# Performance work log

Measured on AMD Instinct MI355X. Metric: run time of the kernel, lower is better.

The kernel has to match this reference:

```python
import jax, jax.numpy as jnp
import numpy as np

B, S, H, DH = 2, 2048, 24, 32
E = H * DH  # 768


def setup_inputs() -> dict:
    key = jax.random.key(0)
    ks = jax.random.split(key, 7)
    embedding = jax.random.normal(ks[0], (B, S, E), dtype=jnp.float32)
    mask = jax.random.randint(ks[1], (B, S, S), 0, 2).astype(bool)
    # per-head QKV weights (applied as x @ W, equivalent param to torch Linear W.T)
    Wq = jax.random.normal(ks[2], (H, DH, DH), dtype=jnp.float32) * 0.05
    Wk = jax.random.normal(ks[3], (H, DH, DH), dtype=jnp.float32) * 0.05
    Wv = jax.random.normal(ks[4], (H, DH, DH), dtype=jnp.float32) * 0.05
    Wo = jax.random.normal(ks[5], (E, E), dtype=jnp.float32) * 0.02
    bo = jax.random.normal(ks[6], (E,), dtype=jnp.float32) * 0.02
    return {"embedding": embedding, "mask": mask, "Wq": Wq, "Wk": Wk,
            "Wv": Wv, "Wo": Wo, "bo": bo}


def reference(embedding, mask, Wq, Wk, Wv, Wo, bo):
    # split channels into heads: [B,S,H,DH]
    xh = embedding.reshape(B, S, H, DH)
    # per-head projections (batched over heads)
    Q = jnp.einsum('bshd,hde->bhse', xh, Wq)
    K = jnp.einsum('bshd,hde->bhse', xh, Wk)
    V = jnp.einsum('bshd,hde->bhse', xh, Wv)
    scale = 1.0 / jnp.sqrt(jnp.float32(DH))
    scores = jnp.einsum('bhqd,bhkd->bhqk', Q, K) * scale
    # faithful quirk: masked positions set to -1e-6 (not -inf)
    scores = jnp.where(mask[:, None, :, :], scores, jnp.float32(-1e-6))
    probs = jax.nn.softmax(scores, axis=-1)
    out = jnp.einsum('bhqk,bhkd->bqhd', probs, V)  # [B,S,H,DH]
    out = out.reshape(B, S, E)  # concat heads along feature dim
    return out @ Wo.T + bo
```

## Files before the change

kernel.cpp:

```cpp
#include <hip/hip_runtime.h>
#include <hip/hip_bf16.h>

#define B_  2
#define S_  2048
#define H_  24
#define DH_ 32
#define E_  768
#define SW_ (S_/32)

#define NB_QKV  ((S_/64)*(B_*H_))
#define NB_MASK ((B_*S_*S_)/256)
#define NB_WO   ((E_*E_)/1024)

typedef __attribute__((ext_vector_type(8))) short short8;
typedef __attribute__((ext_vector_type(4))) float f32x4;
typedef _Float16 half8  __attribute__((ext_vector_type(8)));
typedef _Float16 half2v __attribute__((ext_vector_type(2)));
typedef __fp16   fp16x2 __attribute__((ext_vector_type(2)));

static __device__ __forceinline__ half2v cvt2h(float a, float b) {
    fp16x2 t = __builtin_amdgcn_cvt_pkrtz(a, b);
    return __builtin_bit_cast(half2v, t);
}

static __device__ __forceinline__ short4 pack4(float a, float b, float c, float d) {
    union { __hip_bfloat162 h[2]; short4 s; } u;
    u.h[0] = __float22bfloat162_rn(make_float2(a, b));
    u.h[1] = __float22bfloat162_rn(make_float2(c, d));
    return u.s;
}
static __device__ __forceinline__ short8 pack8f(const float* a, const float* b) {
    union { __hip_bfloat162 h[4]; short8 s; } u;
    u.h[0] = __float22bfloat162_rn(make_float2(a[0], a[1]));
    u.h[1] = __float22bfloat162_rn(make_float2(a[2], a[3]));
    u.h[2] = __float22bfloat162_rn(make_float2(b[0], b[1]));
    u.h[3] = __float22bfloat162_rn(make_float2(b[2], b[3]));
    return u.s;
}
static __device__ __forceinline__ short8 pack8(float4 a, float4 b) {
    union { __hip_bfloat162 h[4]; short8 s; } u;
    u.h[0] = __float22bfloat162_rn(make_float2(a.x, a.y));
    u.h[1] = __float22bfloat162_rn(make_float2(a.z, a.w));
    u.h[2] = __float22bfloat162_rn(make_float2(b.x, b.y));
    u.h[3] = __float22bfloat162_rn(make_float2(b.z, b.w));
    return u.s;
}
static __device__ __forceinline__ short8 wfrag(const float* __restrict__ Wb,
                                               int quad, int eo) {
    float w[8];
#pragma unroll
    for (int j = 0; j < 8; ++j) w[j] = Wb[(quad * 8 + j) * 32 + eo];
    return pack8f(w, w + 4);
}

#define QSCALE  0.25503487f

static __device__ __forceinline__ float mexp2(float s, unsigned mw, int pos) {
    const int m = __builtin_amdgcn_sbfe((int)mw, pos, 1);
    const int xi = __builtin_bit_cast(int, s) & m;
    return __builtin_amdgcn_exp2f(__builtin_bit_cast(float, xi));
}

__global__ __launch_bounds__(256) void prep_qkv_kernel(
    const float* __restrict__ x, const int* __restrict__ mask,
    const float* __restrict__ Wo,
    const float* __restrict__ Wq, const float* __restrict__ Wk,
    const float* __restrict__ Wv,
    __hip_bfloat16* __restrict__ Qo,
    __hip_bfloat16* __restrict__ Ko,
    _Float16* __restrict__ Vto,
    unsigned int* __restrict__ mbits, _Float16* __restrict__ Wob)
{
    const int bx = blockIdx.x;
    if (bx < NB_QKV) {
        const int bh   = bx >> 5;
        const int b    = bh / H_;
        const int h    = bh - b * H_;
        const int wave = threadIdx.x >> 6;
        const int lane = threadIdx.x & 63;
        const int col  = lane & 15;
        const int quad = lane >> 4;
        const int sw   = (bx & 31) * 64 + wave * 16;
        const int s    = sw + col;

        const float* xp = x + ((size_t)b * S_ + s) * E_ + h * DH_ + quad * 8;
        const float4 xa = *reinterpret_cast<const float4*>(xp);
        const float4 xb = *reinterpret_cast<const float4*>(xp + 4);
        const short8 xf = pack8(xa, xb);

        const int wb = h * DH_ * DH_;
        const short8 aQ0 = wfrag(Wq + wb, quad, col);
        const short8 aQ1 = wfrag(Wq + wb, quad, col + 16);
        const short8 aK0 = wfrag(Wk + wb, quad, col);
        const short8 aK1 = wfrag(Wk + wb, quad, col + 16);
        const short8 bV0 = wfrag(Wv + wb, quad, col);
        const short8 bV1 = wfrag(Wv + wb, quad, col + 16);

        const f32x4 z = {0.f, 0.f, 0.f, 0.f};
        const f32x4 qt0 = __builtin_amdgcn_mfma_f32_16x16x32_bf16(aQ0, xf, z, 0, 0, 0);
        const f32x4 qt1 = __builtin_amdgcn_mfma_f32_16x16x32_bf16(aQ1, xf, z, 0, 0, 0);
        const f32x4 kt0 = __builtin_amdgcn_mfma_f32_16x16x32_bf16(aK0, xf, z, 0, 0, 0);
        const f32x4 kt1 = __builtin_amdgcn_mfma_f32_16x16x32_bf16(aK1, xf, z, 0, 0, 0);
        const f32x4 vv0 = __builtin_amdgcn_mfma_f32_16x16x32_bf16(xf, bV0, z, 0, 0, 0);
        const f32x4 vv1 = __builtin_amdgcn_mfma_f32_16x16x32_bf16(xf, bV1, z, 0, 0, 0);

        __hip_bfloat16* qrow = Qo + ((size_t)bh * S_ + s) * DH_;
        *reinterpret_cast<short4*>(qrow + quad * 4) =
            pack4(qt0[0] * QSCALE, qt0[1] * QSCALE, qt0[2] * QSCALE, qt0[3] * QSCALE);
        *reinterpret_cast<short4*>(qrow + 16 + quad * 4) =
            pack4(qt1[0] * QSCALE, qt1[1] * QSCALE, qt1[2] * QSCALE, qt1[3] * QSCALE);

        const int t32  = s & 31;
        const int slot = (s & ~31) | (((t32 >> 2) & 1) << 4)
                       | (((t32 >> 3) << 2) | (t32 & 3));
        __hip_bfloat16* krow = Ko + ((size_t)bh * S_ + slot) * DH_;
        *reinterpret_cast<short4*>(krow + quad * 4)      = pack4(kt0[0], kt0[1], kt0[2], kt0[3]);
        *reinterpret_cast<short4*>(krow + 16 + quad * 4) = pack4(kt1[0], kt1[1], kt1[2], kt1[3]);

        const int sb = sw + quad * 4;
        union { half2v h[2]; uint2 u; } v0u, v1u;
        v0u.h[0] = cvt2h(vv0[0], vv0[1]); v0u.h[1] = cvt2h(vv0[2], vv0[3]);
        v1u.h[0] = cvt2h(vv1[0], vv1[1]); v1u.h[1] = cvt2h(vv1[2], vv1[3]);
        *reinterpret_cast<uint2*>(Vto + ((size_t)bh * DH_ + col) * S_ + sb)      = v0u.u;
        *reinterpret_cast<uint2*>(Vto + ((size_t)bh * DH_ + 16 + col) * S_ + sb) = v1u.u;
    } else if (bx < NB_QKV + NB_MASK) {
        const int idx  = (bx - NB_QKV) * 256 + threadIdx.x;
        const int lane = threadIdx.x & 63;
        const unsigned long long bal = __ballot(mask[idx] != 0);
        if (lane == 0) {
            uint2 w;
            w.x = (unsigned int)(bal & 0xffffffffull);
            w.y = (unsigned int)(bal >> 32);
            *reinterpret_cast<uint2*>(mbits + (idx >> 5)) = w;
        }
    } else {
        const int i = ((bx - NB_QKV - NB_MASK) * 256 + threadIdx.x) * 4;
        const float4 w = *reinterpret_cast<const float4*>(Wo + i);
        union { half2v h[2]; uint2 u; } uu;
        uu.h[0] = cvt2h(w.x, w.y);
        uu.h[1] = cvt2h(w.z, w.w);
        *reinterpret_cast<uint2*>(Wob + i) = uu.u;
    }
}

__global__ __launch_bounds__(64, 3) void attn_kernel(
    const __hip_bfloat16* __restrict__ Q,
    const __hip_bfloat16* __restrict__ K,
    const _Float16* __restrict__ Vt,
    const unsigned int* __restrict__ mbits,
    _Float16* __restrict__ Opart,
    float* __restrict__ lpart,
    int parts)
{
    const int bid  = blockIdx.x;
    const int xcd  = bid & 7;
    const int t_   = bid >> 3;
    const int bh   = xcd * 6 + (t_ % 6);
    const int rest = t_ / 6;
    const int qsub = rest & 31;
    const int part = rest >> 5;

    const int b    = bh / H_;
    const int h    = bh - b * H_;
    const int niter = S_ / (64 * parts);
    const int kbeg  = part * (S_ / parts);
    const int lane = threadIdx.x & 63;
    const int col  = lane & 15;
    const int quad = lane >> 4;
    const int q0   = qsub * 64;

    const __hip_bfloat16* Qbh = Q  + (size_t)bh * S_ * DH_;
    const __hip_bfloat16* Kbh = K  + (size_t)bh * S_ * DH_;
    const _Float16*       Vbh = Vt + (size_t)bh * DH_ * S_;

    short8 qf[4];
#pragma unroll
    for (int t = 0; t < 4; ++t)
        qf[t] = *reinterpret_cast<const short8*>(
            Qbh + (size_t)(q0 + t * 16 + col) * DH_ + quad * 8);

    const _Float16* Vp0 = Vbh + (size_t)col * S_ + kbeg + quad * 8;
    const _Float16* Vp1 = Vbh + (size_t)(16 + col) * S_ + kbeg + quad * 8;

    const __hip_bfloat16* Kf = Kbh + (size_t)(kbeg + col) * DH_ + quad * 8;
    const unsigned int* mbb = mbits + (size_t)b * S_ * SW_ + (kbeg >> 5);
    const unsigned int* mf0 = mbb + (size_t)(q0 +  0 + col) * SW_;
    const unsigned int* mf1 = mbb + (size_t)(q0 + 16 + col) * SW_;
    const unsigned int* mf2 = mbb + (size_t)(q0 + 32 + col) * SW_;
    const unsigned int* mf3 = mbb + (size_t)(q0 + 48 + col) * SW_;

    const int posL = quad * 8;
    const int posH = quad * 8 + 4;

    union { uint4 u; half8 v; } onesu;
    onesu.u = make_uint4(0x3C003C00u, 0x3C003C00u, 0x3C003C00u, 0x3C003C00u);
    const half8 ones_h = onesu.v;

    f32x4 o0a[4], o1a[4], la[4];
#pragma unroll
    for (int t = 0; t < 4; ++t) {
        o0a[t] = (f32x4){0.f,0.f,0.f,0.f};
        o1a[t] = (f32x4){0.f,0.f,0.f,0.f};
        la[t]  = (f32x4){0.f,0.f,0.f,0.f};
    }

    short8 ak0, ak1, ak2, ak3; uint2 am0, am1, am2, am3;
    short8 bk0, bk1, bk2, bk3; uint2 bm0, bm1, bm2, bm3;

    auto load_a = [&]() {
        ak0 = *reinterpret_cast<const short8*>(Kf);
        ak1 = *reinterpret_cast<const short8*>(Kf + 16 * DH_);
        ak2 = *reinterpret_cast<const short8*>(Kf + 32 * DH_);
        ak3 = *reinterpret_cast<const short8*>(Kf + 48 * DH_);
        am0 = *reinterpret_cast<const uint2*>(mf0);
        am1 = *reinterpret_cast<const uint2*>(mf1);
        am2 = *reinterpret_cast<const uint2*>(mf2);
        am3 = *reinterpret_cast<const uint2*>(mf3);
        Kf += 64 * DH_; mf0 += 2; mf1 += 2; mf2 += 2; mf3 += 2;
    };
    auto load_b = [&]() {
        bk0 = *reinterpret_cast<const short8*>(Kf);
        bk1 = *reinterpret_cast<const short8*>(Kf + 16 * DH_);
        bk2 = *reinterpret_cast<const short8*>(Kf + 32 * DH_);
        bk3 = *reinterpret_cast<const short8*>(Kf + 48 * DH_);
        bm0 = *reinterpret_cast<const uint2*>(mf0);
        bm1 = *reinterpret_cast<const uint2*>(mf1);
        bm2 = *reinterpret_cast<const uint2*>(mf2);
        bm3 = *reinterpret_cast<const uint2*>(mf3);
        Kf += 64 * DH_; mf0 += 2; mf1 += 2; mf2 += 2; mf3 += 2;
    };

    auto compute = [&](const short8& kA0, const short8& kA1,
                       const short8& kB0, const short8& kB1,
                       uint2 w0, uint2 w1, uint2 w2, uint2 w3) {
        const half8 vA0 = *reinterpret_cast<const half8*>(Vp0);
        const half8 vA1 = *reinterpret_cast<const half8*>(Vp1);
        const half8 vB0 = *reinterpret_cast<const half8*>(Vp0 + 32);
        const half8 vB1 = *reinterpret_cast<const half8*>(Vp1 + 32);
        const uint2 mw[4] = {w0, w1, w2, w3};
        const f32x4 z = {0.f, 0.f, 0.f, 0.f};

        f32x4 s0[4], s1[4];
#pragma unroll
        for (int t = 0; t < 4; ++t) {
            s0[t] = __builtin_amdgcn_mfma_f32_16x16x32_bf16(kA0, qf[t], z, 0, 0, 0);
            s1[t] = __builtin_amdgcn_mfma_f32_16x16x32_bf16(kA1, qf[t], z, 0, 0, 0);
        }
#pragma unroll
        for (int t = 0; t < 4; ++t) {
            float p0[4], p1[4];
#pragma unroll
            for (int r = 0; r < 4; ++r) {
                p0[r] = mexp2(s0[t][r], mw[t].x, posL + r);
                p1[r] = mexp2(s1[t][r], mw[t].x, posH + r);
            }
            union { half2v h[4]; half8 v; } pu;
            pu.h[0] = cvt2h(p0[0], p0[1]);
            pu.h[1] = cvt2h(p0[2], p0[3]);
            pu.h[2] = cvt2h(p1[0], p1[1]);
            pu.h[3] = cvt2h(p1[2], p1[3]);
            const half8 pf = pu.v;
            o0a[t] = __builtin_amdgcn_mfma_f32_16x16x32_f16(vA0, pf, o0a[t], 0, 0, 0);
            o1a[t] = __builtin_amdgcn_mfma_f32_16x16x32_f16(vA1, pf, o1a[t], 0, 0, 0);
            la[t]  = __builtin_amdgcn_mfma_f32_16x16x32_f16(ones_h, pf, la[t], 0, 0, 0);
        }

#pragma unroll
        for (int t = 0; t < 4; ++t) {
            s0[t] = __builtin_amdgcn_mfma_f32_16x16x32_bf16(kB0, qf[t], z, 0, 0, 0);
            s1[t] = __builtin_amdgcn_mfma_f32_16x16x32_bf16(kB1, qf[t], z, 0, 0, 0);
        }
#pragma unroll
        for (int t = 0; t < 4; ++t) {
            float p0[4], p1[4];
#pragma unroll
            for (int r = 0; r < 4; ++r) {
                p0[r] = mexp2(s0[t][r], mw[t].y, posL + r);
                p1[r] = mexp2(s1[t][r], mw[t].y, posH + r);
            }
            union { half2v h[4]; half8 v; } pu;
            pu.h[0] = cvt2h(p0[0], p0[1]);
            pu.h[1] = cvt2h(p0[2], p0[3]);
            pu.h[2] = cvt2h(p1[0], p1[1]);
            pu.h[3] = cvt2h(p1[2], p1[3]);
            const half8 pf = pu.v;
            o0a[t] = __builtin_amdgcn_mfma_f32_16x16x32_f16(vB0, pf, o0a[t], 0, 0, 0);
            o1a[t] = __builtin_amdgcn_mfma_f32_16x16x32_f16(vB1, pf, o1a[t], 0, 0, 0);
            la[t]  = __builtin_amdgcn_mfma_f32_16x16x32_f16(ones_h, pf, la[t], 0, 0, 0);
        }

        Vp0 += 64;
        Vp1 += 64;
    };

    load_a();
    for (int it = 0; it < niter; it += 2) {
        load_b();
        compute(ak0, ak1, ak2, ak3, am0, am1, am2, am3);
        load_a();
        compute(bk0, bk1, bk2, bk3, bm0, bm1, bm2, bm3);
    }

    _Float16* Ob = Opart + (size_t)part * B_ * S_ * E_;
    float* lp = lpart + (size_t)part * B_ * H_ * S_ + (size_t)bh * S_;
#pragma unroll
    for (int t = 0; t < 4; ++t) {
        union { half2v h[2]; uint2 u; } u0, u1;
        u0.h[0] = cvt2h(o0a[t][0], o0a[t][1]);
        u0.h[1] = cvt2h(o0a[t][2], o0a[t][3]);
        u1.h[0] = cvt2h(o1a[t][0], o1a[t][1]);
        u1.h[1] = cvt2h(o1a[t][2], o1a[t][3]);
        _Float16* orow = Ob + ((size_t)b * S_ + q0 + t * 16 + col) * E_ + h * DH_;
        *reinterpret_cast<uint2*>(orow + quad * 4)      = u0.u;
        *reinterpret_cast<uint2*>(orow + 16 + quad * 4) = u1.u;
        if (quad == 0) lp[q0 + t * 16 + col] = la[t][0];
    }
}

template <int PARTS>
__global__ __launch_bounds__(256) void proj_kernel(
    const _Float16* __restrict__ Opart,
    const float* __restrict__ lpart,
    const _Float16* __restrict__ Wob,
    const float* __restrict__ bo,
    float* __restrict__ out)
{
    const int wave = threadIdx.x >> 6;
    const int lane = threadIdx.x & 63;
    const int col  = lane & 15;
    const int quad = lane >> 4;
    const int m0   = blockIdx.x * 16;
    const int n0   = blockIdx.y * 256 + wave * 64;

    const int m = m0 + col;
    const int b = m / S_;
    const int s = m - b * S_;
    const float* lpb = lpart + (size_t)(b * H_) * S_ + s;

    f32x4 acc[4] = {{0.f,0.f,0.f,0.f},{0.f,0.f,0.f,0.f},
                    {0.f,0.f,0.f,0.f},{0.f,0.f,0.f,0.f}};
    for (int k0 = 0; k0 < E_; k0 += 32) {
        const int h = k0 >> 5;
        const size_t aofs = (size_t)m * E_ + k0 + quad * 8;

        float l = 0.f;
#pragma unroll
        for (int pp = 0; pp < PARTS; ++pp)
            l += lpb[(size_t)pp * B_ * H_ * S_ + (size_t)h * S_];
        const float linv = __builtin_amdgcn_rcpf(l);
        const half2v lv = cvt2h(linv, linv);

        union UA { uint4 u; half2v h[4]; half8 v; } ua;
        ua.u = *reinterpret_cast<const uint4*>(Opart + aofs);
#pragma unroll
        for (int pp = 1; pp < PARTS; ++pp) {
            union UA ub;
            ub.u = *reinterpret_cast<const uint4*>(
                Opart + (size_t)pp * B_ * S_ * E_ + aofs);
#pragma unroll
            for (int i = 0; i < 4; ++i) ua.h[i] += ub.h[i];
        }
#pragma unroll
        for (int i = 0; i < 4; ++i) ua.h[i] *= lv;
        const half8 af = ua.v;

#pragma unroll
        for (int j = 0; j < 4; ++j) {
            union UA wb;
            wb.u = *reinterpret_cast<const uint4*>(
                Wob + (size_t)(n0 + j * 16 + col) * E_ + k0 + quad * 8);
            acc[j] = __builtin_amdgcn_mfma_f32_16x16x32_f16(af, wb.v, acc[j], 0, 0, 0);
        }
    }
#pragma unroll
    for (int j = 0; j < 4; ++j) {
        const int n = n0 + j * 16 + col;
        const float bias = bo[n];
#pragma unroll
        for (int r = 0; r < 4; ++r) {
            const int mm = m0 + quad * 4 + r;
            out[(size_t)mm * E_ + n] = acc[j][r] + bias;
        }
    }
}

extern "C" void kernel_launch(void* const* d_in, const int* in_sizes, int n_in,
                              void* d_out, int out_size, void* d_ws, size_t ws_size,
                              hipStream_t stream)
{
    const float* emb = (const float*)d_in[0];
    const int*   msk = (const int*)d_in[1];
    const float* Wq  = (const float*)d_in[2];
    const float* Wk  = (const float*)d_in[3];
    const float* Wv  = (const float*)d_in[4];
    const float* Wo  = (const float*)d_in[5];
    const float* bo  = (const float*)d_in[6];
    float* out = (float*)d_out;

    const size_t nqkv = (size_t)B_ * H_ * S_ * DH_;
    char* p = (char*)d_ws;
    __hip_bfloat16* Q    = (__hip_bfloat16*)p;  p += nqkv * 2;
    __hip_bfloat16* Kp   = (__hip_bfloat16*)p;  p += nqkv * 2;
    _Float16*      Vt    = (_Float16*)p;        p += nqkv * 2;
    unsigned int*  mbits = (unsigned int*)p;    p += (size_t)B_ * S_ * SW_ * 4;
    _Float16*      Wob   = (_Float16*)p;        p += (size_t)E_ * E_ * 2;
    _Float16*      Op    = (_Float16*)p;
    const size_t base = (size_t)(p - (char*)d_ws);

    int parts = 1;
    {
        const size_t need = base + (size_t)2 * nqkv * 2
                          + (size_t)2 * B_ * H_ * S_ * 4;
        if (ws_size >= need) parts = 2;
    }
    float* lpart = (float*)(Op + (size_t)parts * nqkv);

    prep_qkv_kernel<<<NB_QKV + NB_MASK + NB_WO, 256, 0, stream>>>(
        emb, msk, Wo, Wq, Wk, Wv, Q, Kp, Vt, mbits, Wob);
    attn_kernel<<<1536 * parts, 64, 0, stream>>>(
        Q, Kp, Vt, mbits, Op, lpart, parts);
    if (parts == 2)
        proj_kernel<2><<<dim3((B_ * S_) / 16, E_ / 256), 256, 0, stream>>>(
            Op, lpart, Wob, bo, out);
    else
        proj_kernel<1><<<dim3((B_ * S_) / 16, E_ / 256), 256, 0, stream>>>(
            Op, lpart, Wob, bo, out);
}
```

Baseline: 217.4 us.

## Batch mask packing per wave, double-buffer proj loads, allow four KV splits

The mask-packing path now has each wave ballot four rows of a 64-column chunk instead of one, so there are four times fewer blocks and each thread keeps more loads in flight. The output projection loop is software-pipelined with two register buffers, so the next k-slice's Opart, l and Wo loads are issued before the current MFMAs run. The host also picks four KV partitions when the workspace is large enough, which gives attention more parallelism. In exchange the projection reads and reduces more partial outputs and uses more registers.

```diff
diff --git a/kernel.cpp b/kernel.cpp
--- a/kernel.cpp
+++ b/kernel.cpp
@@ -9,7 +9,7 @@
 #define SW_ (S_/32)
 
 #define NB_QKV  ((S_/64)*(B_*H_))
-#define NB_MASK ((B_*S_*S_)/256)
+#define NB_MSK4 ((B_*S_*S_)/1024)
 #define NB_WO   ((E_*E_)/1024)
 
 typedef __attribute__((ext_vector_type(8))) short short8;
@@ -123,18 +123,30 @@
         v1u.h[0] = cvt2h(vv1[0], vv1[1]); v1u.h[1] = cvt2h(vv1[2], vv1[3]);
         *reinterpret_cast<uint2*>(Vto + ((size_t)bh * DH_ + col) * S_ + sb)      = v0u.u;
         *reinterpret_cast<uint2*>(Vto + ((size_t)bh * DH_ + 16 + col) * S_ + sb) = v1u.u;
-    } else if (bx < NB_QKV + NB_MASK) {
-        const int idx  = (bx - NB_QKV) * 256 + threadIdx.x;
+    } else if (bx < NB_QKV + NB_MSK4) {
+        const int wid  = (bx - NB_QKV) * 4 + (threadIdx.x >> 6);
         const int lane = threadIdx.x & 63;
-        const unsigned long long bal = __ballot(mask[idx] != 0);
-        if (lane == 0) {
-            uint2 w;
-            w.x = (unsigned int)(bal & 0xffffffffull);
-            w.y = (unsigned int)(bal >> 32);
-            *reinterpret_cast<uint2*>(mbits + (idx >> 5)) = w;
+        const int rg   = wid >> 5;
+        const int kc   = wid & 31;
+        const int row0 = rg * 4;
+        const int k    = kc * 64 + lane;
+        int mv[4];
+#pragma unroll
+        for (int j = 0; j < 4; ++j)
+            mv[j] = mask[(size_t)(row0 + j) * S_ + k];
+#pragma unroll
+        for (int j = 0; j < 4; ++j) {
+            const unsigned long long bal = __ballot(mv[j] != 0);
+            if (lane == 0) {
+                uint2 w;
+                w.x = (unsigned int)(bal & 0xffffffffull);
+                w.y = (unsigned int)(bal >> 32);
+                *reinterpret_cast<uint2*>(
+                    mbits + (size_t)(row0 + j) * SW_ + kc * 2) = w;
+            }
         }
     } else {
-        const int i = ((bx - NB_QKV - NB_MASK) * 256 + threadIdx.x) * 4;
+        const int i = ((bx - NB_QKV - NB_MSK4) * 256 + threadIdx.x) * 4;
         const float4 w = *reinterpret_cast<const float4*>(Wo + i);
         union { half2v h[2]; uint2 u; } uu;
         uu.h[0] = cvt2h(w.x, w.y);
@@ -336,42 +348,88 @@
     const int b = m / S_;
     const int s = m - b * S_;
     const float* lpb = lpart + (size_t)(b * H_) * S_ + s;
+    const size_t BHS = (size_t)B_ * H_ * S_;
+    const size_t BSE = (size_t)B_ * S_ * E_;
+
+    union UA { uint4 u; half2v h[4]; half8 v; };
 
     f32x4 acc[4] = {{0.f,0.f,0.f,0.f},{0.f,0.f,0.f,0.f},
                     {0.f,0.f,0.f,0.f},{0.f,0.f,0.f,0.f}};
-    for (int k0 = 0; k0 < E_; k0 += 32) {
+
+    float lA[PARTS]; UA oA[PARTS]; UA wA[4];
+    float lB[PARTS]; UA oB[PARTS]; UA wB[4];
+
+    auto load_a = [&](int k0) {
         const int h = k0 >> 5;
         const size_t aofs = (size_t)m * E_ + k0 + quad * 8;
-
+#pragma unroll
+        for (int pp = 0; pp < PARTS; ++pp) {
+            lA[pp] = lpb[(size_t)pp * BHS + (size_t)h * S_];
+            oA[pp].u = *reinterpret_cast<const uint4*>(
+                Opart + (size_t)pp * BSE + aofs);
+        }
+#pragma unroll
+        for (int j = 0; j < 4; ++j)
+            wA[j].u = *reinterpret_cast<const uint4*>(
+                Wob + (size_t)(n0 + j * 16 + col) * E_ + k0 + quad * 8);
+    };
+    auto load_b = [&](int k0) {
+        const int h = k0 >> 5;
+        const size_t aofs = (size_t)m * E_ + k0 + quad * 8;
+#pragma unroll
+        for (int pp = 0; pp < PARTS; ++pp) {
+            lB[pp] = lpb[(size_t)pp * BHS + (size_t)h * S_];
+            oB[pp].u = *reinterpret_cast<const uint4*>(
+                Opart + (size_t)pp * BSE + aofs);
+        }
+#pragma unroll
+        for (int j = 0; j < 4; ++j)
+            wB[j].u = *reinterpret_cast<const uint4*>(
+                Wob + (size_t)(n0 + j * 16 + col) * E_ + k0 + quad * 8);
+    };
+    auto comp_a = [&]() {
         float l = 0.f;
 #pragma unroll
-        for (int pp = 0; pp < PARTS; ++pp)
-            l += lpb[(size_t)pp * B_ * H_ * S_ + (size_t)h * S_];
+        for (int pp = 0; pp < PARTS; ++pp) l += lA[pp];
         const float linv = __builtin_amdgcn_rcpf(l);
         const half2v lv = cvt2h(linv, linv);
-
-        union UA { uint4 u; half2v h[4]; half8 v; } ua;
-        ua.u = *reinterpret_cast<const uint4*>(Opart + aofs);
-#pragma unroll
-        for (int pp = 1; pp < PARTS; ++pp) {
-            union UA ub;
-            ub.u = *reinterpret_cast<const uint4*>(
-                Opart + (size_t)pp * B_ * S_ * E_ + aofs);
-#pragma unroll
-            for (int i = 0; i < 4; ++i) ua.h[i] += ub.h[i];
-        }
+        UA ua = oA[0];
+#pragma unroll
+        for (int pp = 1; pp < PARTS; ++pp)
+#pragma unroll
+            for (int i = 0; i < 4; ++i) ua.h[i] += oA[pp].h[i];
 #pragma unroll
         for (int i = 0; i < 4; ++i) ua.h[i] *= lv;
-        const half8 af = ua.v;
-
-#pragma unroll
-        for (int j = 0; j < 4; ++j) {
-            union UA wb;
-            wb.u = *reinterpret_cast<const uint4*>(
-                Wob + (size_t)(n0 + j * 16 + col) * E_ + k0 + quad * 8);
-            acc[j] = __builtin_amdgcn_mfma_f32_16x16x32_f16(af, wb.v, acc[j], 0, 0, 0);
-        }
-    }
+#pragma unroll
+        for (int j = 0; j < 4; ++j)
+            acc[j] = __builtin_amdgcn_mfma_f32_16x16x32_f16(ua.v, wA[j].v, acc[j], 0, 0, 0);
+    };
+    auto comp_b = [&]() {
+        float l = 0.f;
+#pragma unroll
+        for (int pp = 0; pp < PARTS; ++pp) l += lB[pp];
+        const float linv = __builtin_amdgcn_rcpf(l);
+        const half2v lv = cvt2h(linv, linv);
+        UA ua = oB[0];
+#pragma unroll
+        for (int pp = 1; pp < PARTS; ++pp)
+#pragma unroll
+            for (int i = 0; i < 4; ++i) ua.h[i] += oB[pp].h[i];
+#pragma unroll
+        for (int i = 0; i < 4; ++i) ua.h[i] *= lv;
+#pragma unroll
+        for (int j = 0; j < 4; ++j)
+            acc[j] = __builtin_amdgcn_mfma_f32_16x16x32_f16(ua.v, wB[j].v, acc[j], 0, 0, 0);
+    };
+
+    load_a(0);
+    for (int k0 = 0; k0 < E_; k0 += 64) {
+        load_b(k0 + 32);
+        comp_a();
+        if (k0 + 64 < E_) load_a(k0 + 64);
+        comp_b();
+    }
+
 #pragma unroll
     for (int j = 0; j < 4; ++j) {
         const int n = n0 + j * 16 + col;
@@ -407,19 +465,20 @@
     _Float16*      Op    = (_Float16*)p;
     const size_t base = (size_t)(p - (char*)d_ws);
 
+    const size_t per_part = (size_t)nqkv * 2 + (size_t)B_ * H_ * S_ * 4;
     int parts = 1;
-    {
-        const size_t need = base + (size_t)2 * nqkv * 2
-                          + (size_t)2 * B_ * H_ * S_ * 4;
-        if (ws_size >= need) parts = 2;
-    }
+    if (ws_size >= base + 4 * per_part)      parts = 4;
+    else if (ws_size >= base + 2 * per_part) parts = 2;
     float* lpart = (float*)(Op + (size_t)parts * nqkv);
 
-    prep_qkv_kernel<<<NB_QKV + NB_MASK + NB_WO, 256, 0, stream>>>(
+    prep_qkv_kernel<<<NB_QKV + NB_MSK4 + NB_WO, 256, 0, stream>>>(
         emb, msk, Wo, Wq, Wk, Wv, Q, Kp, Vt, mbits, Wob);
     attn_kernel<<<1536 * parts, 64, 0, stream>>>(
         Q, Kp, Vt, mbits, Op, lpart, parts);
-    if (parts == 2)
+    if (parts == 4)
+        proj_kernel<4><<<dim3((B_ * S_) / 16, E_ / 256), 256, 0, stream>>>(
+            Op, lpart, Wob, bo, out);
+    else if (parts == 2)
         proj_kernel<2><<<dim3((B_ * S_) / 16, E_ / 256), 256, 0, stream>>>(
             Op, lpart, Wob, bo, out);
     else
```

Measured after the change: 225.5 us. 1.04x slower.
